# Optimization experiments

Hardware: AMD Instinct MI355X
Metric: run time of the kernel (lower is better)

The kernel has to match this reference:

```python
import jax, jax.numpy as jnp
import numpy as np


def _conv2d(x, w, b):
    # 3x3 conv, stride 1, pad 1, NCHW
    y = jax.lax.conv_general_dilated(x, w, (1, 1), ((1, 1), (1, 1)),
                                     dimension_numbers=('NCHW', 'OIHW', 'NCHW'))
    return y + b[None, :, None, None]


def _up2(x):
    return jnp.repeat(jnp.repeat(x, 2, axis=2), 2, axis=3)


def _mdconv(x, w, b, ow, ob):
    # Modulated deformable conv v2 (mmcv semantics): 3x3, stride 1, pad 1,
    # dilation 1, deformable_groups=1. Offsets/mask predicted by conv_offset,
    # out = chunk3 -> (o1, o2, mask); offset = cat(o1, o2); mask = sigmoid(mask).
    B, Cin, H, W = x.shape
    off = _conv2d(x, ow, ob)                        # [B,27,H,W]
    o1, o2, m = jnp.split(off, 3, axis=1)
    offs = jnp.concatenate([o1, o2], axis=1)        # [B,18,H,W]
    dy, dx = offs[:, 0::2], offs[:, 1::2]           # [B,9,H,W] (dy,dx interleaved per kernel pt)
    mask = jax.nn.sigmoid(m)                        # [B,9,H,W]
    ky, kx = jnp.meshgrid(jnp.arange(3), jnp.arange(3), indexing='ij')
    # sampling positions: p0 + pn + offset (pad=1)
    py = jnp.arange(H, dtype=x.dtype)[None, None, :, None] - 1.0 + ky.reshape(1, 9, 1, 1) + dy
    px = jnp.arange(W, dtype=x.dtype)[None, None, None, :] - 1.0 + kx.reshape(1, 9, 1, 1) + dx
    y0 = jnp.floor(py); x0 = jnp.floor(px)
    wy1 = py - y0; wx1 = px - x0
    y0i = y0.astype(jnp.int32); x0i = x0.astype(jnp.int32)
    flat = x.reshape(B, Cin, H * W)

    def gather(yi, xi):
        valid = ((yi >= 0) & (yi < H) & (xi >= 0) & (xi < W)).astype(x.dtype)  # zero padding
        idx = jnp.clip(yi, 0, H - 1) * W + jnp.clip(xi, 0, W - 1)             # [B,9,H,W]
        g = jax.vmap(lambda f, i: f[:, i])(flat, idx)                          # [B,Cin,9,H,W]
        return g * valid[:, None]

    val = (gather(y0i, x0i) * ((1 - wy1) * (1 - wx1))[:, None]
           + gather(y0i, x0i + 1) * ((1 - wy1) * wx1)[:, None]
           + gather(y0i + 1, x0i) * (wy1 * (1 - wx1))[:, None]
           + gather(y0i + 1, x0i + 1) * (wy1 * wx1)[:, None])
    cols = val * mask[:, None]                      # [B,Cin,9,H,W]
    out = jnp.einsum('ock,bckhw->bohw', w.reshape(w.shape[0], Cin, 9), cols)
    return out + b[None, :, None, None]


def setup_inputs() -> dict:
    key = jax.random.key(0)
    ks = jax.random.split(key, 24)
    C = 256
    sizes = [(96, 96), (48, 48), (24, 24), (12, 12)]
    d = {}
    for i, (h, w) in enumerate(sizes):
        d[f'x{i}'] = jax.random.normal(ks[i], (2, C, h, w), dtype=jnp.float32)
    for i in range(4):
        d[f'w{i}'] = jax.random.normal(ks[4 + i], (C, C, 3, 3), dtype=jnp.float32) * 0.02
        d[f'b{i}'] = jax.random.normal(ks[8 + i], (C,), dtype=jnp.float32) * 0.02
    for i in range(1, 4):
        d[f'ow{i}'] = jax.random.normal(ks[12 + i], (27, C, 3, 3), dtype=jnp.float32) * 0.01
        d[f'ob{i}'] = jax.random.normal(ks[16 + i], (27,), dtype=jnp.float32) * 0.01
    return d


def reference(x0, x1, x2, x3, w0, w1, w2, w3, b0, b1, b2, b3,
              ow1, ow2, ow3, ob1, ob2, ob3):
    # tdm_convs[3] called with level=1 -> deform; the same-size nearest interpolate is identity
    t3 = _mdconv(x3, w3, b3, ow3, ob3)
    # i=3: tdm_convs[2](2, x2 + up(t3)) -> deform
    t2 = _mdconv(x2 + _up2(t3), w2, b2, ow2, ob2)
    # i=2: tdm_convs[1](1, x1 + up(t2)) -> deform
    t1 = _mdconv(x1 + _up2(t2), w1, b1, ow1, ob1)
    # i=1: tdm_convs[0](0, x0 + up(t1)) -> level 0 < start_level -> plain conv
    t0 = _conv2d(x0 + _up2(t1), w0, b0)
    return (t0, t1, t2, t3)
```

## Files before the change

### kernel.cpp

```cpp
#include <hip/hip_runtime.h>
#include <math.h>

__device__ __forceinline__ ushort f2bf(float f) {
    unsigned int u = __float_as_uint(f);
    u += 0x7FFFu + ((u >> 16) & 1u);
    return (ushort)(u >> 16);
}

typedef __attribute__((address_space(1))) const unsigned int guint;
typedef __attribute__((address_space(3))) unsigned int luint;
__device__ __forceinline__ void gload_lds16(const void* g, void* l) {
    __builtin_amdgcn_global_load_lds((guint*)g, (luint*)l, 16, 0, 0);
}

template<int N>
__device__ __forceinline__ void waitvm() {
    if constexpr (N == 0)      asm volatile("s_waitcnt vmcnt(0)" ::: "memory");
    else if constexpr (N == 4) asm volatile("s_waitcnt vmcnt(4)" ::: "memory");
    else                       asm volatile("s_waitcnt vmcnt(6)" ::: "memory");
}

using bfrag = __attribute__((ext_vector_type(8))) short;
using f4    = __attribute__((ext_vector_type(4))) float;

__device__ __forceinline__ void bf8_to_f(uint4 v, float* o) {
    unsigned int u[4] = {v.x, v.y, v.z, v.w};
    #pragma unroll
    for (int i = 0; i < 4; ++i) {
        o[2 * i]     = __uint_as_float(u[i] << 16);
        o[2 * i + 1] = __uint_as_float(u[i] & 0xFFFF0000u);
    }
}

__device__ __forceinline__ void xs_body(void* smem,
    const float* __restrict__ x, const float* __restrict__ prev,
    ushort* __restrict__ xs, int H, int W, int bx, int by, int bz)
{
    ushort (*tile)[72] = (ushort(*)[72])smem;
    const int HW = H * W, W2 = W >> 1;
    int b = bz, c0 = by * 32, hw0 = bx * 64;
    const float* xb = x + ((size_t)b * 256 + c0) * HW;
    const float* pb = prev ? prev + ((size_t)b * 256 + c0) * (HW >> 2) : nullptr;

    int hwl = threadIdx.x & 63, cl0 = threadIdx.x >> 6;
    int hw = hw0 + hwl;
    bool ok = hw < HW;
    int hwc = ok ? hw : HW - 1;
    int h = hwc / W, w = hwc - h * W;
    int pidx = (h >> 1) * W2 + (w >> 1);
    #pragma unroll
    for (int p = 0; p < 8; ++p) {
        int cl = p * 4 + cl0;
        float v = 0.f;
        if (ok) {
            v = xb[(size_t)cl * HW + hw];
            if (pb) v += pb[(size_t)cl * (HW >> 2) + pidx];
        }
        tile[cl][hwl] = f2bf(v);
    }
    __syncthreads();
    int hwl2 = threadIdx.x >> 2, cc = (threadIdx.x & 3) * 8;
    int hw2 = hw0 + hwl2;
    if (hw2 < HW) {
        ushort vals[8];
        #pragma unroll
        for (int j = 0; j < 8; ++j) vals[j] = tile[cc + j][hwl2];
        *(uint4*)&xs[((size_t)b * HW + hw2) * 256 + c0 + cc] = *(uint4*)vals;
    }
}

struct ProArgs {
    const float* wsrc[7];
    ushort*      wdst[7];
    float*       outp[3];
    const float* bias[3];
    int          HW[3];
    float*       zbase;
    int          z4;
    const float* x3;
    ushort*      xs3;
};
__global__ __launch_bounds__(256) void prolog_kernel(ProArgs a) {
    __shared__ __align__(16) char smem[32 * 72 * 2];
    int y = blockIdx.y;
    if (y < 7) {
        int M = (y < 4) ? 256 : 27;
        int idx = blockIdx.x * 256 + threadIdx.x;
        if (idx < M * 288) {
            int m = idx / 288, rem = idx - m * 288;
            int r = rem >> 5, c8 = rem & 31;
            const float* s = a.wsrc[y] + ((size_t)(m * 256 + c8 * 8)) * 9 + r;
            ushort vals[8];
            #pragma unroll
            for (int j = 0; j < 8; ++j) vals[j] = f2bf(s[j * 9]);
            *(uint4*)&a.wdst[y][(size_t)m * 2304 + r * 256 + c8 * 8] = *(uint4*)vals;
        }
    } else if (y < 10) {
        int t = y - 7;
        int HW = a.HW[t];
        int i = blockIdx.x * 256 + threadIdx.x;
        if (i < 128 * HW) {
            int e = i << 2;
            int m = (e / HW) & 255;
            float v = a.bias[t][m];
            *(float4*)&a.outp[t][e] = float4{v, v, v, v};
        }
    } else if (y == 10) {
        int i = blockIdx.x * 256 + threadIdx.x;
        if (i < a.z4) ((float4*)a.zbase)[i] = float4{0.f, 0.f, 0.f, 0.f};
    } else {
        int vb = blockIdx.x;
        if (vb < 48)
            xs_body(smem, a.x3, nullptr, a.xs3, 12, 12, vb % 3, (vb / 3) & 7, vb / 24);
    }
}

__global__ __launch_bounds__(256) void xs_nhwc(
    const float* __restrict__ x, const float* __restrict__ prev,
    ushort* __restrict__ xs, int H, int W)
{
    __shared__ __align__(16) char smem[32 * 72 * 2];
    xs_body(smem, x, prev, xs, H, W, blockIdx.x, blockIdx.y, blockIdx.z);
}

__global__ __launch_bounds__(256) void off_mfma(
    const ushort* __restrict__ A, const ushort* __restrict__ xs,
    const ushort* __restrict__ zeros, float* __restrict__ offbuf,
    int N, int H, int W, int ktiles)
{
    __shared__ __align__(16) ushort As[2][32 * 32];
    __shared__ __align__(16) ushort Bs[2][64 * 32];
    const int b  = blockIdx.z;
    const int n0 = blockIdx.x * 64;
    const int kt0 = blockIdx.y * ktiles * 32;
    const int tid = threadIdx.x, lane = tid & 63, wv = tid >> 6;
    const ushort* xb = xs + (size_t)b * N * 256;

    int n = n0 + (tid >> 2); if (n >= N) n = N - 1;
    int h = n / W, w = n - h * W;
    int kcc = (tid & 3) * 8;

    auto stage = [&](int kt, int bi) {
        int r = kt >> 8, c0k = kt & 255;
        int ry = r / 3 - 1, rx = r - (r / 3) * 3 - 1;
        if (tid < 128) {
            int row = tid >> 2; if (row > 26) row = 26;
            gload_lds16(A + (size_t)row * 2304 + kt + kcc,
                        (char*)As[bi] + (size_t)(tid & ~63) * 16);
        }
        int ih = h + ry, iw = w + rx;
        const ushort* src = (ih >= 0 && ih < H && iw >= 0 && iw < W)
            ? xb + (((size_t)(ih * W + iw)) << 8) + c0k + kcc
            : zeros;
        gload_lds16(src, (char*)Bs[bi] + (size_t)(tid & ~63) * 16);
    };

    f4 acc[2] = {};
    stage(kt0, 0);
    for (int kk = 0; kk < ktiles; ++kk) {
        __syncthreads();
        if (kk + 1 < ktiles) stage(kt0 + (kk + 1) * 32, (kk + 1) & 1);
        const ushort* as = As[kk & 1];
        const ushort* bs = Bs[kk & 1];
        bfrag bf = *(const bfrag*)&bs[(wv * 16 + (lane & 15)) * 32 + (lane >> 4) * 8];
        bfrag a0 = *(const bfrag*)&as[(lane & 15) * 32 + (lane >> 4) * 8];
        bfrag a1 = *(const bfrag*)&as[(16 + (lane & 15)) * 32 + (lane >> 4) * 8];
        acc[0] = __builtin_amdgcn_mfma_f32_16x16x32_bf16(a0, bf, acc[0], 0, 0, 0);
        acc[1] = __builtin_amdgcn_mfma_f32_16x16x32_bf16(a1, bf, acc[1], 0, 0, 0);
    }

    int nn = n0 + wv * 16 + (lane & 15);
    if (nn < N) {
        #pragma unroll
        for (int mb = 0; mb < 2; ++mb)
            #pragma unroll
            for (int t = 0; t < 4; ++t) {
                int m = mb * 16 + (lane >> 4) * 4 + t;
                if (m < 27)
                    atomicAdd(&offbuf[((size_t)b * 27 + m) * N + nn], acc[mb][t]);
            }
    }
}

__global__ __launch_bounds__(256) void sampling_kernel(
    const ushort* __restrict__ xs, const float* __restrict__ off,
    const float* __restrict__ ob, ushort* __restrict__ cols,
    int H, int W)
{
    __shared__ float4 gw[8][9];
    __shared__ int4   go[8][9];
    const int HW = H * W;
    const int b = blockIdx.z;
    const int hw0 = blockIdx.x * 8;
    const int tid = threadIdx.x;
    const float* offb = off + (size_t)b * 27 * HW;
    const ushort* xb = xs + (size_t)b * HW * 256;

    if (tid < 72) {
        int hwl = tid / 9, k = tid - hwl * 9;
        int hw = hw0 + hwl; if (hw >= HW) hw = HW - 1;
        int h = hw / W, w = hw - h * W;
        float dy = offb[(size_t)(2 * k) * HW + hw] + ob[2 * k];
        float dx = offb[(size_t)(2 * k + 1) * HW + hw] + ob[2 * k + 1];
        float mv = offb[(size_t)(18 + k) * HW + hw] + ob[18 + k];
        float mk = 1.0f / (1.0f + __expf(-mv));
        float py = (float)h - 1.0f + (float)(k / 3) + dy;
        float px = (float)w - 1.0f + (float)(k % 3) + dx;
        float y0f = floorf(py), x0f = floorf(px);
        float wy = py - y0f, wx = px - x0f;
        int y0 = (int)y0f, x0i = (int)x0f;
        int y1 = y0 + 1, x1 = x0i + 1;
        bool vy0 = (y0 >= 0) & (y0 < H), vy1 = (y1 >= 0) & (y1 < H);
        bool vx0 = (x0i >= 0) & (x0i < W), vx1 = (x1 >= 0) & (x1 < W);
        float w00 = (1.f - wy) * (1.f - wx) * ((vy0 & vx0) ? mk : 0.f);
        float w01 = (1.f - wy) * wx        * ((vy0 & vx1) ? mk : 0.f);
        float w10 = wy * (1.f - wx)        * ((vy1 & vx0) ? mk : 0.f);
        float w11 = wy * wx                * ((vy1 & vx1) ? mk : 0.f);
        int cy0 = min(max(y0, 0), H - 1), cy1 = min(max(y1, 0), H - 1);
        int cx0 = min(max(x0i, 0), W - 1), cx1 = min(max(x1, 0), W - 1);
        gw[hwl][k] = float4{w00, w01, w10, w11};
        go[hwl][k] = int4{(cy0 * W + cx0) << 8, (cy0 * W + cx1) << 8,
                          (cy1 * W + cx0) << 8, (cy1 * W + cx1) << 8};
    }
    __syncthreads();

    int hwl = tid >> 5, cb = (tid & 31) * 8;
    int hw = hw0 + hwl;
    if (hw >= HW) return;
    ushort* colp = cols + ((size_t)b * HW + hw) * 2304 + cb;

    #pragma unroll
    for (int k = 0; k < 9; ++k) {
        float4 wv = gw[hwl][k];
        int4   ov = go[hwl][k];
        float f00[8], f01[8], f10[8], f11[8];
        bf8_to_f(*(const uint4*)(xb + ov.x + cb), f00);
        bf8_to_f(*(const uint4*)(xb + ov.y + cb), f01);
        bf8_to_f(*(const uint4*)(xb + ov.z + cb), f10);
        bf8_to_f(*(const uint4*)(xb + ov.w + cb), f11);
        unsigned int pk[4];
        #pragma unroll
        for (int t = 0; t < 4; ++t) {
            float lo = f00[2 * t] * wv.x + f01[2 * t] * wv.y +
                       f10[2 * t] * wv.z + f11[2 * t] * wv.w;
            float hi = f00[2 * t + 1] * wv.x + f01[2 * t + 1] * wv.y +
                       f10[2 * t + 1] * wv.z + f11[2 * t + 1] * wv.w;
            pk[t] = (unsigned int)f2bf(lo) | ((unsigned int)f2bf(hi) << 16);
        }
        *(uint4*)(colp + k * 256) = make_uint4(pk[0], pk[1], pk[2], pk[3]);
    }
}

template<bool IMPLICIT, bool SPLITK, int BM>
__global__ __launch_bounds__(256) void mfma_gemm(
    const ushort* __restrict__ A, const float* __restrict__ bias,
    const ushort* __restrict__ Bt, const ushort* __restrict__ zeros,
    float* __restrict__ outp, int N, int H, int W, int kchunk)
{
    constexpr int MT = 256 / BM;
    constexpr int AL = BM / 32;
    constexpr int AI = BM / 32;
    constexpr int S  = AL + 2;
    __shared__ __align__(16) ushort As[2][BM * 64];
    __shared__ __align__(16) ushort Bs[2][64 * 64];
    const int b  = blockIdx.z;
    const int m0 = (blockIdx.y % MT) * BM;
    const int kt0 = (blockIdx.y / MT) * kchunk;
    const int n0 = blockIdx.x * 64;
    const int tid  = threadIdx.x;
    const int lane = tid & 63;
    const int wv   = tid >> 6;
    const int wm = wv & 1, wn = wv >> 1;

    const ushort* Bb = IMPLICIT ? Bt + (size_t)b * N * 256
                                : Bt + (size_t)b * (size_t)N * 2304;

    const int sc8 = ((tid & 7) ^ ((tid >> 3) & 7)) * 8;
    const int srow = tid >> 3;
    int bn[2], bh[2], bw[2];
    #pragma unroll
    for (int j = 0; j < 2; ++j) {
        int n = n0 + j * 32 + srow; if (n >= N) n = N - 1;
        bn[j] = n; bh[j] = n / W; bw[j] = n - bh[j] * W;
    }

    auto stage = [&](int kt, int bi) {
        #pragma unroll
        for (int i = 0; i < AL; ++i) {
            gload_lds16(A + (size_t)(m0 + i * 32 + srow) * 2304 + kt + sc8,
                        (char*)As[bi] + (size_t)(i * 256 + (tid & ~63)) * 16);
        }
        if (!IMPLICIT) {
            #pragma unroll
            for (int j = 0; j < 2; ++j)
                gload_lds16(Bb + (size_t)bn[j] * 2304 + kt + sc8,
                            (char*)Bs[bi] + (size_t)(j * 256 + (tid & ~63)) * 16);
        } else {
            int r = kt >> 8, c0k = kt & 255;
            int ry = r / 3 - 1, rx = r - (r / 3) * 3 - 1;
            #pragma unroll
            for (int j = 0; j < 2; ++j) {
                int ih = bh[j] + ry, iw = bw[j] + rx;
                const ushort* src = (ih >= 0 && ih < H && iw >= 0 && iw < W)
                    ? Bb + (((size_t)(ih * W + iw)) << 8) + c0k + sc8
                    : zeros;
                gload_lds16(src, (char*)Bs[bi] + (size_t)(j * 256 + (tid & ~63)) * 16);
            }
        }
    };

    const int fq = (lane >> 4);
    const int fv = (lane & 7);
    f4 acc[AI][2] = {};

    const int nit = kchunk >> 6;
    stage(kt0, 0);
    if (nit > 1) stage(kt0 + 64, 1);
    for (int it = 0; it < nit; ++it) {
        if (it + 1 < nit) waitvm<S>(); else waitvm<0>();
        __builtin_amdgcn_s_barrier();
        __builtin_amdgcn_sched_barrier(0);
        const ushort* as = As[it & 1];
        const ushort* bs = Bs[it & 1];
        bfrag af[2][AI], bf[2][2];
        #pragma unroll
        for (int kh = 0; kh < 2; ++kh) {
            int ch = ((kh * 4 + fq) ^ fv) * 8;
            #pragma unroll
            for (int i = 0; i < AI; ++i)
                af[kh][i] = *(const bfrag*)&as[(wm * (BM / 2) + i * 16 + (lane & 15)) * 64 + ch];
            #pragma unroll
            for (int j = 0; j < 2; ++j)
                bf[kh][j] = *(const bfrag*)&bs[(wn * 32 + j * 16 + (lane & 15)) * 64 + ch];
        }
        asm volatile("s_waitcnt lgkmcnt(0)" ::: "memory");
        __builtin_amdgcn_s_barrier();
        __builtin_amdgcn_sched_barrier(0);
        if (it + 2 < nit) stage(kt0 + (it + 2) * 64, it & 1);
        #pragma unroll
        for (int kh = 0; kh < 2; ++kh)
            #pragma unroll
            for (int i = 0; i < AI; ++i)
                #pragma unroll
                for (int j = 0; j < 2; ++j)
                    acc[i][j] = __builtin_amdgcn_mfma_f32_16x16x32_bf16(
                        af[kh][i], bf[kh][j], acc[i][j], 0, 0, 0);
    }

    const int mb = m0 + wm * (BM / 2), nb = n0 + wn * 32;
    #pragma unroll
    for (int i = 0; i < AI; ++i) {
        int mrow = mb + i * 16 + (lane >> 4) * 4;
        #pragma unroll
        for (int j = 0; j < 2; ++j) {
            int n = nb + j * 16 + (lane & 15);
            if (n < N) {
                #pragma unroll
                for (int t = 0; t < 4; ++t) {
                    int m = mrow + t;
                    if (SPLITK)
                        atomicAdd(&outp[((size_t)b * 256 + m) * N + n], acc[i][j][t]);
                    else
                        outp[((size_t)b * 256 + m) * N + n] = acc[i][j][t] + bias[m];
                }
            }
        }
    }
}

extern "C" void kernel_launch(void* const* d_in, const int* in_sizes, int n_in,
                              void* d_out, int out_size, void* d_ws, size_t ws_size,
                              hipStream_t stream)
{
    const float* x[4]   = {(const float*)d_in[0], (const float*)d_in[1],
                           (const float*)d_in[2], (const float*)d_in[3]};
    const float* wgt[4] = {(const float*)d_in[4], (const float*)d_in[6],
                           (const float*)d_in[8], (const float*)d_in[10]};
    const float* bia[4] = {(const float*)d_in[5], (const float*)d_in[7],
                           (const float*)d_in[9], (const float*)d_in[11]};
    const float* owt[4] = {nullptr, (const float*)d_in[12],
                           (const float*)d_in[14], (const float*)d_in[16]};
    const float* obv[4] = {nullptr, (const float*)d_in[13],
                           (const float*)d_in[15], (const float*)d_in[17]};

    const int B = 2;
    const int Hs[4] = {96, 48, 24, 12};
    const int HWs[4] = {96 * 96, 48 * 48, 24 * 24, 12 * 12};

    float* out = (float*)d_out;
    size_t outOff[4];
    outOff[0] = 0;
    outOff[1] = outOff[0] + (size_t)B * 256 * HWs[0];
    outOff[2] = outOff[1] + (size_t)B * 256 * HWs[1];
    outOff[3] = outOff[2] + (size_t)B * 256 * HWs[2];

    char* ws = (char*)d_ws;
    size_t off = 0;
    auto carve = [&](size_t bytes) { void* p = ws + off; off = (off + bytes + 255) & ~(size_t)255; return p; };
    ushort* wbf[4];
    ushort* owbf[4] = {nullptr, nullptr, nullptr, nullptr};
    for (int i = 0; i < 4; ++i) wbf[i] = (ushort*)carve((size_t)256 * 2304 * 2);
    for (int i = 1; i < 4; ++i) owbf[i] = (ushort*)carve((size_t)27 * 2304 * 2);
    ushort* cols = (ushort*)carve((size_t)B * HWs[1] * 2304 * 2);
    ushort* xsb[4];
    for (int i = 0; i < 4; ++i) xsb[i] = (ushort*)carve((size_t)B * 256 * HWs[i] * 2);
    int offElems = B * 27 * (HWs[1] + HWs[2] + HWs[3]);
    float* offbase = (float*)carve((size_t)offElems * 4 + 1024);
    ushort* zeros = (ushort*)(offbase + offElems);
    float* offbuf[4] = {nullptr,
                        offbase,
                        offbase + (size_t)B * 27 * HWs[1],
                        offbase + (size_t)B * 27 * (HWs[1] + HWs[2])};

    {
        ProArgs a;
        a.wsrc[0] = wgt[0]; a.wsrc[1] = wgt[1]; a.wsrc[2] = wgt[2]; a.wsrc[3] = wgt[3];
        a.wsrc[4] = owt[1]; a.wsrc[5] = owt[2]; a.wsrc[6] = owt[3];
        a.wdst[0] = wbf[0]; a.wdst[1] = wbf[1]; a.wdst[2] = wbf[2]; a.wdst[3] = wbf[3];
        a.wdst[4] = owbf[1]; a.wdst[5] = owbf[2]; a.wdst[6] = owbf[3];
        for (int i = 0; i < 3; ++i) {
            a.outp[i] = out + outOff[i + 1]; a.bias[i] = bia[i + 1]; a.HW[i] = HWs[i + 1];
        }
        a.zbase = offbase;
        a.z4 = (offElems * 4 + 1024) / 16;
        a.x3 = x[3];
        a.xs3 = xsb[3];
        dim3 grd(1152, 12);
        prolog_kernel<<<grd, 256, 0, stream>>>(a);
    }

    const int ktiles[4] = {0, 9, 6, 3};
    const int ksplit[4] = {1, 4, 6, 12};

    for (int lvl = 3; lvl >= 1; --lvl) {
        int H = Hs[lvl], W = H, HW = HWs[lvl];

        {
            dim3 grd((HW + 63) / 64, 72 / ktiles[lvl], B);
            off_mfma<<<grd, 256, 0, stream>>>(
                owbf[lvl], xsb[lvl], zeros, offbuf[lvl], HW, H, W, ktiles[lvl]);
        }
        {
            dim3 grd((HW + 7) / 8, 1, B);
            sampling_kernel<<<grd, 256, 0, stream>>>(
                xsb[lvl], offbuf[lvl], obv[lvl], cols, H, W);
        }
        {
            dim3 grd((HW + 63) / 64, 4 * ksplit[lvl], B);
            mfma_gemm<false, true, 64><<<grd, 256, 0, stream>>>(
                wbf[lvl], bia[lvl], cols, zeros, out + outOff[lvl],
                HW, H, W, 2304 / ksplit[lvl]);
        }
        {
            int Hn = Hs[lvl - 1];
            dim3 grd((HWs[lvl - 1] + 63) / 64, 8, B);
            xs_nhwc<<<grd, 256, 0, stream>>>(
                x[lvl - 1], out + outOff[lvl], xsb[lvl - 1], Hn, Hn);
        }
    }

    {
        dim3 grd((HWs[0] + 63) / 64, 2, 2);
        mfma_gemm<true, false, 128><<<grd, 256, 0, stream>>>(
            wbf[0], bia[0], xsb[0], zeros, out + outOff[0],
            HWs[0], Hs[0], Hs[0], 2304);
    }
}
```

Baseline: 252.5 us.

## Fuse all stages into one persistent kernel with software grid barriers

Replaces the chain of about thirteen kernel launches (prolog, then offset, sampling, GEMM and layout conversion per level, then the final conv) with a single persistent kernel of 512 blocks. Stages are separated by atomic-counter grid barriers and each block walks the virtual blocks of a stage in a grid-stride loop. Each level also gets its own cols buffer. The aim is to remove launch gaps and tail idle time between the small per-level stages. In exchange every stage boundary becomes a full grid barrier, the shared-memory footprint is fixed at 48 KB, and the final conv runs on a capped grid of 512 blocks. The barrier assumes all 512 blocks are co-resident, which launch_bounds(256,2) should allow on this GPU.

```diff
diff --git a/kernel.cpp b/kernel.cpp
--- a/kernel.cpp
+++ b/kernel.cpp
@@ -1,5 +1,7 @@
 #include <hip/hip_runtime.h>
 #include <math.h>
+
+constexpr int GRID = 512;
 
 __device__ __forceinline__ ushort f2bf(float f) {
     unsigned int u = __float_as_uint(f);
@@ -30,6 +32,18 @@
         o[2 * i]     = __uint_as_float(u[i] << 16);
         o[2 * i + 1] = __uint_as_float(u[i] & 0xFFFF0000u);
     }
+}
+
+__device__ __forceinline__ void gsync(unsigned int* cnt, unsigned int target) {
+    __syncthreads();
+    if (threadIdx.x == 0) {
+        __threadfence();
+        __hip_atomic_fetch_add(cnt, 1u, __ATOMIC_RELAXED, __HIP_MEMORY_SCOPE_AGENT);
+        while (__hip_atomic_load(cnt, __ATOMIC_RELAXED, __HIP_MEMORY_SCOPE_AGENT) < target)
+            __builtin_amdgcn_s_sleep(2);
+        __threadfence();
+    }
+    __syncthreads();
 }
 
 __device__ __forceinline__ void xs_body(void* smem,
@@ -69,72 +83,17 @@
     }
 }
 
-struct ProArgs {
-    const float* wsrc[7];
-    ushort*      wdst[7];
-    float*       outp[3];
-    const float* bias[3];
-    int          HW[3];
-    float*       zbase;
-    int          z4;
-    const float* x3;
-    ushort*      xs3;
-};
-__global__ __launch_bounds__(256) void prolog_kernel(ProArgs a) {
-    __shared__ __align__(16) char smem[32 * 72 * 2];
-    int y = blockIdx.y;
-    if (y < 7) {
-        int M = (y < 4) ? 256 : 27;
-        int idx = blockIdx.x * 256 + threadIdx.x;
-        if (idx < M * 288) {
-            int m = idx / 288, rem = idx - m * 288;
-            int r = rem >> 5, c8 = rem & 31;
-            const float* s = a.wsrc[y] + ((size_t)(m * 256 + c8 * 8)) * 9 + r;
-            ushort vals[8];
-            #pragma unroll
-            for (int j = 0; j < 8; ++j) vals[j] = f2bf(s[j * 9]);
-            *(uint4*)&a.wdst[y][(size_t)m * 2304 + r * 256 + c8 * 8] = *(uint4*)vals;
-        }
-    } else if (y < 10) {
-        int t = y - 7;
-        int HW = a.HW[t];
-        int i = blockIdx.x * 256 + threadIdx.x;
-        if (i < 128 * HW) {
-            int e = i << 2;
-            int m = (e / HW) & 255;
-            float v = a.bias[t][m];
-            *(float4*)&a.outp[t][e] = float4{v, v, v, v};
-        }
-    } else if (y == 10) {
-        int i = blockIdx.x * 256 + threadIdx.x;
-        if (i < a.z4) ((float4*)a.zbase)[i] = float4{0.f, 0.f, 0.f, 0.f};
-    } else {
-        int vb = blockIdx.x;
-        if (vb < 48)
-            xs_body(smem, a.x3, nullptr, a.xs3, 12, 12, vb % 3, (vb / 3) & 7, vb / 24);
-    }
-}
-
-__global__ __launch_bounds__(256) void xs_nhwc(
-    const float* __restrict__ x, const float* __restrict__ prev,
-    ushort* __restrict__ xs, int H, int W)
-{
-    __shared__ __align__(16) char smem[32 * 72 * 2];
-    xs_body(smem, x, prev, xs, H, W, blockIdx.x, blockIdx.y, blockIdx.z);
-}
-
-__global__ __launch_bounds__(256) void off_mfma(
+__device__ __forceinline__ void do_off(char* smem,
     const ushort* __restrict__ A, const ushort* __restrict__ xs,
     const ushort* __restrict__ zeros, float* __restrict__ offbuf,
-    int N, int H, int W, int ktiles)
+    int N, int H, int W, int ktiles, int bx, int by, int bz)
 {
-    __shared__ __align__(16) ushort As[2][32 * 32];
-    __shared__ __align__(16) ushort Bs[2][64 * 32];
-    const int b  = blockIdx.z;
-    const int n0 = blockIdx.x * 64;
-    const int kt0 = blockIdx.y * ktiles * 32;
+    ushort* As0 = (ushort*)smem;
+    ushort* Bs0 = (ushort*)(smem + 4096);
+    const int n0 = bx * 64;
+    const int kt0 = by * ktiles * 32;
     const int tid = threadIdx.x, lane = tid & 63, wv = tid >> 6;
-    const ushort* xb = xs + (size_t)b * N * 256;
+    const ushort* xb = xs + (size_t)bz * N * 256;
 
     int n = n0 + (tid >> 2); if (n >= N) n = N - 1;
     int h = n / W, w = n - h * W;
@@ -146,13 +105,13 @@
         if (tid < 128) {
             int row = tid >> 2; if (row > 26) row = 26;
             gload_lds16(A + (size_t)row * 2304 + kt + kcc,
-                        (char*)As[bi] + (size_t)(tid & ~63) * 16);
+                        (char*)(As0 + bi * 1024) + (size_t)(tid & ~63) * 16);
         }
         int ih = h + ry, iw = w + rx;
         const ushort* src = (ih >= 0 && ih < H && iw >= 0 && iw < W)
             ? xb + (((size_t)(ih * W + iw)) << 8) + c0k + kcc
             : zeros;
-        gload_lds16(src, (char*)Bs[bi] + (size_t)(tid & ~63) * 16);
+        gload_lds16(src, (char*)(Bs0 + bi * 2048) + (size_t)(tid & ~63) * 16);
     };
 
     f4 acc[2] = {};
@@ -160,8 +119,8 @@
     for (int kk = 0; kk < ktiles; ++kk) {
         __syncthreads();
         if (kk + 1 < ktiles) stage(kt0 + (kk + 1) * 32, (kk + 1) & 1);
-        const ushort* as = As[kk & 1];
-        const ushort* bs = Bs[kk & 1];
+        const ushort* as = As0 + (kk & 1) * 1024;
+        const ushort* bs = Bs0 + (kk & 1) * 2048;
         bfrag bf = *(const bfrag*)&bs[(wv * 16 + (lane & 15)) * 32 + (lane >> 4) * 8];
         bfrag a0 = *(const bfrag*)&as[(lane & 15) * 32 + (lane >> 4) * 8];
         bfrag a1 = *(const bfrag*)&as[(16 + (lane & 15)) * 32 + (lane >> 4) * 8];
@@ -177,24 +136,23 @@
             for (int t = 0; t < 4; ++t) {
                 int m = mb * 16 + (lane >> 4) * 4 + t;
                 if (m < 27)
-                    atomicAdd(&offbuf[((size_t)b * 27 + m) * N + nn], acc[mb][t]);
+                    atomicAdd(&offbuf[((size_t)bz * 27 + m) * N + nn], acc[mb][t]);
             }
     }
 }
 
-__global__ __launch_bounds__(256) void sampling_kernel(
+__device__ __forceinline__ void do_samp(char* smem,
     const ushort* __restrict__ xs, const float* __restrict__ off,
     const float* __restrict__ ob, ushort* __restrict__ cols,
-    int H, int W)
+    int H, int W, int bx, int bz)
 {
-    __shared__ float4 gw[8][9];
-    __shared__ int4   go[8][9];
+    float4 (*gw)[9] = (float4(*)[9])smem;
+    int4   (*go)[9] = (int4(*)[9])(smem + 8 * 9 * 16);
     const int HW = H * W;
-    const int b = blockIdx.z;
-    const int hw0 = blockIdx.x * 8;
+    const int hw0 = bx * 8;
     const int tid = threadIdx.x;
-    const float* offb = off + (size_t)b * 27 * HW;
-    const ushort* xb = xs + (size_t)b * HW * 256;
+    const float* offb = off + (size_t)bz * 27 * HW;
+    const ushort* xb = xs + (size_t)bz * HW * 256;
 
     if (tid < 72) {
         int hwl = tid / 9, k = tid - hwl * 9;
@@ -226,54 +184,54 @@
 
     int hwl = tid >> 5, cb = (tid & 31) * 8;
     int hw = hw0 + hwl;
-    if (hw >= HW) return;
-    ushort* colp = cols + ((size_t)b * HW + hw) * 2304 + cb;
-
-    #pragma unroll
-    for (int k = 0; k < 9; ++k) {
-        float4 wv = gw[hwl][k];
-        int4   ov = go[hwl][k];
-        float f00[8], f01[8], f10[8], f11[8];
-        bf8_to_f(*(const uint4*)(xb + ov.x + cb), f00);
-        bf8_to_f(*(const uint4*)(xb + ov.y + cb), f01);
-        bf8_to_f(*(const uint4*)(xb + ov.z + cb), f10);
-        bf8_to_f(*(const uint4*)(xb + ov.w + cb), f11);
-        unsigned int pk[4];
-        #pragma unroll
-        for (int t = 0; t < 4; ++t) {
-            float lo = f00[2 * t] * wv.x + f01[2 * t] * wv.y +
-                       f10[2 * t] * wv.z + f11[2 * t] * wv.w;
-            float hi = f00[2 * t + 1] * wv.x + f01[2 * t + 1] * wv.y +
-                       f10[2 * t + 1] * wv.z + f11[2 * t + 1] * wv.w;
-            pk[t] = (unsigned int)f2bf(lo) | ((unsigned int)f2bf(hi) << 16);
-        }
-        *(uint4*)(colp + k * 256) = make_uint4(pk[0], pk[1], pk[2], pk[3]);
+    if (hw < HW) {
+        ushort* colp = cols + ((size_t)bz * HW + hw) * 2304 + cb;
+        #pragma unroll
+        for (int k = 0; k < 9; ++k) {
+            float4 wv = gw[hwl][k];
+            int4   ov = go[hwl][k];
+            float f00[8], f01[8], f10[8], f11[8];
+            bf8_to_f(*(const uint4*)(xb + ov.x + cb), f00);
+            bf8_to_f(*(const uint4*)(xb + ov.y + cb), f01);
+            bf8_to_f(*(const uint4*)(xb + ov.z + cb), f10);
+            bf8_to_f(*(const uint4*)(xb + ov.w + cb), f11);
+            unsigned int pk[4];
+            #pragma unroll
+            for (int t = 0; t < 4; ++t) {
+                float lo = f00[2 * t] * wv.x + f01[2 * t] * wv.y +
+                           f10[2 * t] * wv.z + f11[2 * t] * wv.w;
+                float hi = f00[2 * t + 1] * wv.x + f01[2 * t + 1] * wv.y +
+                           f10[2 * t + 1] * wv.z + f11[2 * t + 1] * wv.w;
+                pk[t] = (unsigned int)f2bf(lo) | ((unsigned int)f2bf(hi) << 16);
+            }
+            *(uint4*)(colp + k * 256) = make_uint4(pk[0], pk[1], pk[2], pk[3]);
+        }
     }
 }
 
 template<bool IMPLICIT, bool SPLITK, int BM>
-__global__ __launch_bounds__(256) void mfma_gemm(
+__device__ __forceinline__ void do_gemm(char* smem,
     const ushort* __restrict__ A, const float* __restrict__ bias,
     const ushort* __restrict__ Bt, const ushort* __restrict__ zeros,
-    float* __restrict__ outp, int N, int H, int W, int kchunk)
+    float* __restrict__ outp, int N, int H, int W, int kchunk,
+    int bx, int by, int bz)
 {
     constexpr int MT = 256 / BM;
     constexpr int AL = BM / 32;
     constexpr int AI = BM / 32;
     constexpr int S  = AL + 2;
-    __shared__ __align__(16) ushort As[2][BM * 64];
-    __shared__ __align__(16) ushort Bs[2][64 * 64];
-    const int b  = blockIdx.z;
-    const int m0 = (blockIdx.y % MT) * BM;
-    const int kt0 = (blockIdx.y / MT) * kchunk;
-    const int n0 = blockIdx.x * 64;
+    ushort* As0 = (ushort*)smem;
+    ushort* Bs0 = (ushort*)(smem + (size_t)BM * 256);
+    const int m0 = (by % MT) * BM;
+    const int kt0 = (by / MT) * kchunk;
+    const int n0 = bx * 64;
     const int tid  = threadIdx.x;
     const int lane = tid & 63;
     const int wv   = tid >> 6;
     const int wm = wv & 1, wn = wv >> 1;
 
-    const ushort* Bb = IMPLICIT ? Bt + (size_t)b * N * 256
-                                : Bt + (size_t)b * (size_t)N * 2304;
+    const ushort* Bb = IMPLICIT ? Bt + (size_t)bz * N * 256
+                                : Bt + (size_t)bz * (size_t)N * 2304;
 
     const int sc8 = ((tid & 7) ^ ((tid >> 3) & 7)) * 8;
     const int srow = tid >> 3;
@@ -288,13 +246,13 @@
         #pragma unroll
         for (int i = 0; i < AL; ++i) {
             gload_lds16(A + (size_t)(m0 + i * 32 + srow) * 2304 + kt + sc8,
-                        (char*)As[bi] + (size_t)(i * 256 + (tid & ~63)) * 16);
+                        (char*)(As0 + bi * BM * 64) + (size_t)(i * 256 + (tid & ~63)) * 16);
         }
         if (!IMPLICIT) {
             #pragma unroll
             for (int j = 0; j < 2; ++j)
                 gload_lds16(Bb + (size_t)bn[j] * 2304 + kt + sc8,
-                            (char*)Bs[bi] + (size_t)(j * 256 + (tid & ~63)) * 16);
+                            (char*)(Bs0 + bi * 64 * 64) + (size_t)(j * 256 + (tid & ~63)) * 16);
         } else {
             int r = kt >> 8, c0k = kt & 255;
             int ry = r / 3 - 1, rx = r - (r / 3) * 3 - 1;
@@ -304,7 +262,7 @@
                 const ushort* src = (ih >= 0 && ih < H && iw >= 0 && iw < W)
                     ? Bb + (((size_t)(ih * W + iw)) << 8) + c0k + sc8
                     : zeros;
-                gload_lds16(src, (char*)Bs[bi] + (size_t)(j * 256 + (tid & ~63)) * 16);
+                gload_lds16(src, (char*)(Bs0 + bi * 64 * 64) + (size_t)(j * 256 + (tid & ~63)) * 16);
             }
         }
     };
@@ -320,8 +278,8 @@
         if (it + 1 < nit) waitvm<S>(); else waitvm<0>();
         __builtin_amdgcn_s_barrier();
         __builtin_amdgcn_sched_barrier(0);
-        const ushort* as = As[it & 1];
-        const ushort* bs = Bs[it & 1];
+        const ushort* as = As0 + (it & 1) * BM * 64;
+        const ushort* bs = Bs0 + (it & 1) * 64 * 64;
         bfrag af[2][AI], bf[2][2];
         #pragma unroll
         for (int kh = 0; kh < 2; ++kh) {
@@ -359,13 +317,128 @@
                 for (int t = 0; t < 4; ++t) {
                     int m = mrow + t;
                     if (SPLITK)
-                        atomicAdd(&outp[((size_t)b * 256 + m) * N + n], acc[i][j][t]);
+                        atomicAdd(&outp[((size_t)bz * 256 + m) * N + n], acc[i][j][t]);
                     else
-                        outp[((size_t)b * 256 + m) * N + n] = acc[i][j][t] + bias[m];
+                        outp[((size_t)bz * 256 + m) * N + n] = acc[i][j][t] + bias[m];
                 }
             }
         }
     }
+}
+
+struct MegaArgs {
+    const float* wsrc[7];
+    ushort*      wdst[7];
+    float*       out[4];
+    const float* bias[4];
+    const float* x[4];
+    ushort*      xsb[4];
+    const float* obv[4];
+    ushort*      cols[4];
+    float*       offbuf[4];
+    const ushort* zeros;
+    float*       zbase;
+    int          z4;
+    unsigned int* cnt;
+};
+
+__global__ __launch_bounds__(256, 2) void mega_kernel(MegaArgs a) {
+    __shared__ __align__(16) char smem[49152];
+    const int tid = threadIdx.x;
+    unsigned int s = 0;
+
+    for (int vb = blockIdx.x; vb < 2965; vb += GRID) {
+        if (vb < 1245) {
+            const float* src; ushort* dst; int M, base;
+            if (vb < 1152) { int y = vb / 288; src = a.wsrc[y]; dst = a.wdst[y]; M = 256; base = vb - y * 288; }
+            else { int t = (vb - 1152) / 31; src = a.wsrc[4 + t]; dst = a.wdst[4 + t]; M = 27; base = (vb - 1152) - t * 31; }
+            int idx = base * 256 + tid;
+            if (idx < M * 288) {
+                int m = idx / 288, rem = idx - m * 288;
+                int r = rem >> 5, c8 = rem & 31;
+                const float* sp = src + ((size_t)(m * 256 + c8 * 8)) * 9 + r;
+                ushort vals[8];
+                #pragma unroll
+                for (int j = 0; j < 8; ++j) vals[j] = f2bf(sp[j * 9]);
+                *(uint4*)&dst[(size_t)m * 2304 + r * 256 + c8 * 8] = *(uint4*)vals;
+            }
+        } else if (vb < 2757) {
+            float* op; const float* bp; int HW, base;
+            if (vb < 2397)      { op = a.out[1]; bp = a.bias[1]; HW = 2304; base = vb - 1245; }
+            else if (vb < 2685) { op = a.out[2]; bp = a.bias[2]; HW = 576;  base = vb - 2397; }
+            else                { op = a.out[3]; bp = a.bias[3]; HW = 144;  base = vb - 2685; }
+            int i = base * 256 + tid;
+            if (i < 128 * HW) {
+                int e = i << 2;
+                int m = (e / HW) & 255;
+                float v = bp[m];
+                *(float4*)&op[e] = float4{v, v, v, v};
+            }
+        } else if (vb < 2917) {
+            int i = (vb - 2757) * 256 + tid;
+            if (i < a.z4) ((float4*)a.zbase)[i] = float4{0.f, 0.f, 0.f, 0.f};
+        } else {
+            int v = vb - 2917;
+            xs_body(smem, a.x[3], nullptr, a.xsb[3], 12, 12, v % 3, (v / 3) & 7, v / 24);
+            __syncthreads();
+        }
+    }
+    gsync(a.cnt, ++s * GRID);
+
+    for (int vb = blockIdx.x; vb < 144; vb += GRID)
+        do_off(smem, a.wdst[6], a.xsb[3], a.zeros, a.offbuf[3], 144, 12, 12, 3,
+               vb % 3, (vb / 3) % 24, vb / 72);
+    gsync(a.cnt, ++s * GRID);
+    for (int vb = blockIdx.x; vb < 36; vb += GRID)
+        do_samp(smem, a.xsb[3], a.offbuf[3], a.obv[3], a.cols[3], 12, 12, vb % 18, vb / 18);
+    gsync(a.cnt, ++s * GRID);
+    for (int vb = blockIdx.x; vb < 288; vb += GRID)
+        do_gemm<false, true, 64>(smem, a.wdst[3], a.bias[3], a.cols[3], a.zeros, a.out[3],
+                                 144, 12, 12, 192, vb % 3, (vb / 3) % 48, vb / 144);
+    gsync(a.cnt, ++s * GRID);
+    for (int vb = blockIdx.x; vb < 144; vb += GRID) {
+        xs_body(smem, a.x[2], a.out[3], a.xsb[2], 24, 24, vb % 9, (vb / 9) % 8, vb / 72);
+        __syncthreads();
+    }
+    gsync(a.cnt, ++s * GRID);
+
+    for (int vb = blockIdx.x; vb < 216; vb += GRID)
+        do_off(smem, a.wdst[5], a.xsb[2], a.zeros, a.offbuf[2], 576, 24, 24, 6,
+               vb % 9, (vb / 9) % 12, vb / 108);
+    gsync(a.cnt, ++s * GRID);
+    for (int vb = blockIdx.x; vb < 144; vb += GRID)
+        do_samp(smem, a.xsb[2], a.offbuf[2], a.obv[2], a.cols[2], 24, 24, vb % 72, vb / 72);
+    gsync(a.cnt, ++s * GRID);
+    for (int vb = blockIdx.x; vb < 432; vb += GRID)
+        do_gemm<false, true, 64>(smem, a.wdst[2], a.bias[2], a.cols[2], a.zeros, a.out[2],
+                                 576, 24, 24, 384, vb % 9, (vb / 9) % 24, vb / 216);
+    gsync(a.cnt, ++s * GRID);
+    for (int vb = blockIdx.x; vb < 576; vb += GRID) {
+        xs_body(smem, a.x[1], a.out[2], a.xsb[1], 48, 48, vb % 36, (vb / 36) % 8, vb / 288);
+        __syncthreads();
+    }
+    gsync(a.cnt, ++s * GRID);
+
+    for (int vb = blockIdx.x; vb < 576; vb += GRID)
+        do_off(smem, a.wdst[4], a.xsb[1], a.zeros, a.offbuf[1], 2304, 48, 48, 9,
+               vb % 36, (vb / 36) % 8, vb / 288);
+    gsync(a.cnt, ++s * GRID);
+    for (int vb = blockIdx.x; vb < 576; vb += GRID)
+        do_samp(smem, a.xsb[1], a.offbuf[1], a.obv[1], a.cols[1], 48, 48, vb % 288, vb / 288);
+    gsync(a.cnt, ++s * GRID);
+    for (int vb = blockIdx.x; vb < 1152; vb += GRID)
+        do_gemm<false, true, 64>(smem, a.wdst[1], a.bias[1], a.cols[1], a.zeros, a.out[1],
+                                 2304, 48, 48, 576, vb % 36, (vb / 36) % 16, vb / 576);
+    gsync(a.cnt, ++s * GRID);
+    for (int vb = blockIdx.x; vb < 2304; vb += GRID) {
+        xs_body(smem, a.x[0], a.out[1], a.xsb[0], 96, 96, vb % 144, (vb / 144) % 8, vb / 1152);
+        __syncthreads();
+    }
+    gsync(a.cnt, ++s * GRID);
+
+    for (int vb = blockIdx.x; vb < 576; vb += GRID)
+        do_gemm<true, false, 128>(smem, a.wdst[0], a.bias[0], a.xsb[0], a.zeros, a.out[0],
+                                  9216, 96, 96, 2304, vb % 144, (vb / 144) % 2, vb / 288);
 }
 
 extern "C" void kernel_launch(void* const* d_in, const int* in_sizes, int n_in,
@@ -384,7 +457,6 @@
                            (const float*)d_in[15], (const float*)d_in[17]};
 
     const int B = 2;
-    const int Hs[4] = {96, 48, 24, 12};
     const int HWs[4] = {96 * 96, 48 * 48, 24 * 24, 12 * 12};
 
     float* out = (float*)d_out;
@@ -401,7 +473,8 @@
     ushort* owbf[4] = {nullptr, nullptr, nullptr, nullptr};
     for (int i = 0; i < 4; ++i) wbf[i] = (ushort*)carve((size_t)256 * 2304 * 2);
     for (int i = 1; i < 4; ++i) owbf[i] = (ushort*)carve((size_t)27 * 2304 * 2);
-    ushort* cols = (ushort*)carve((size_t)B * HWs[1] * 2304 * 2);
+    ushort* cols[4] = {nullptr, nullptr, nullptr, nullptr};
+    for (int i = 1; i < 4; ++i) cols[i] = (ushort*)carve((size_t)B * HWs[i] * 2304 * 2);
     ushort* xsb[4];
     for (int i = 0; i < 4; ++i) xsb[i] = (ushort*)carve((size_t)B * 256 * HWs[i] * 2);
     int offElems = B * 27 * (HWs[1] + HWs[2] + HWs[3]);
@@ -411,58 +484,28 @@
                         offbase,
                         offbase + (size_t)B * 27 * HWs[1],
                         offbase + (size_t)B * 27 * (HWs[1] + HWs[2])};
-
-    {
-        ProArgs a;
-        a.wsrc[0] = wgt[0]; a.wsrc[1] = wgt[1]; a.wsrc[2] = wgt[2]; a.wsrc[3] = wgt[3];
-        a.wsrc[4] = owt[1]; a.wsrc[5] = owt[2]; a.wsrc[6] = owt[3];
-        a.wdst[0] = wbf[0]; a.wdst[1] = wbf[1]; a.wdst[2] = wbf[2]; a.wdst[3] = wbf[3];
-        a.wdst[4] = owbf[1]; a.wdst[5] = owbf[2]; a.wdst[6] = owbf[3];
-        for (int i = 0; i < 3; ++i) {
-            a.outp[i] = out + outOff[i + 1]; a.bias[i] = bia[i + 1]; a.HW[i] = HWs[i + 1];
-        }
-        a.zbase = offbase;
-        a.z4 = (offElems * 4 + 1024) / 16;
-        a.x3 = x[3];
-        a.xs3 = xsb[3];
-        dim3 grd(1152, 12);
-        prolog_kernel<<<grd, 256, 0, stream>>>(a);
-    }
-
-    const int ktiles[4] = {0, 9, 6, 3};
-    const int ksplit[4] = {1, 4, 6, 12};
-
-    for (int lvl = 3; lvl >= 1; --lvl) {
-        int H = Hs[lvl], W = H, HW = HWs[lvl];
-
-        {
-            dim3 grd((HW + 63) / 64, 72 / ktiles[lvl], B);
-            off_mfma<<<grd, 256, 0, stream>>>(
-                owbf[lvl], xsb[lvl], zeros, offbuf[lvl], HW, H, W, ktiles[lvl]);
-        }
-        {
-            dim3 grd((HW + 7) / 8, 1, B);
-            sampling_kernel<<<grd, 256, 0, stream>>>(
-                xsb[lvl], offbuf[lvl], obv[lvl], cols, H, W);
-        }
-        {
-            dim3 grd((HW + 63) / 64, 4 * ksplit[lvl], B);
-            mfma_gemm<false, true, 64><<<grd, 256, 0, stream>>>(
-                wbf[lvl], bia[lvl], cols, zeros, out + outOff[lvl],
-                HW, H, W, 2304 / ksplit[lvl]);
-        }
-        {
-            int Hn = Hs[lvl - 1];
-            dim3 grd((HWs[lvl - 1] + 63) / 64, 8, B);
-            xs_nhwc<<<grd, 256, 0, stream>>>(
-                x[lvl - 1], out + outOff[lvl], xsb[lvl - 1], Hn, Hn);
-        }
-    }
-
-    {
-        dim3 grd((HWs[0] + 63) / 64, 2, 2);
-        mfma_gemm<true, false, 128><<<grd, 256, 0, stream>>>(
-            wbf[0], bia[0], xsb[0], zeros, out + outOff[0],
-            HWs[0], Hs[0], Hs[0], 2304);
-    }
-}
+    unsigned int* cnt = (unsigned int*)carve(256);
+
+    hipMemsetAsync(cnt, 0, sizeof(unsigned int), stream);
+
+    MegaArgs a;
+    a.wsrc[0] = wgt[0]; a.wsrc[1] = wgt[1]; a.wsrc[2] = wgt[2]; a.wsrc[3] = wgt[3];
+    a.wsrc[4] = owt[1]; a.wsrc[5] = owt[2]; a.wsrc[6] = owt[3];
+    a.wdst[0] = wbf[0]; a.wdst[1] = wbf[1]; a.wdst[2] = wbf[2]; a.wdst[3] = wbf[3];
+    a.wdst[4] = owbf[1]; a.wdst[5] = owbf[2]; a.wdst[6] = owbf[3];
+    for (int i = 0; i < 4; ++i) {
+        a.out[i]  = out + outOff[i];
+        a.bias[i] = bia[i];
+        a.x[i]    = x[i];
+        a.xsb[i]  = xsb[i];
+        a.obv[i]  = obv[i];
+        a.cols[i] = cols[i];
+        a.offbuf[i] = offbuf[i];
+    }
+    a.zeros = zeros;
+    a.zbase = offbase;
+    a.z4 = (offElems * 4 + 1024) / 16;
+    a.cnt = cnt;
+
+    mega_kernel<<<dim3(GRID), 256, 0, stream>>>(a);
+}
```

Result: slower. 874.8 us (+246.4%).
